# Optimization experiments

Measured on AMD Instinct MI355X. Metric: run time of the kernel, lower is better.

Reference implementation:

```python
import jax, jax.numpy as jnp
import numpy as np

GROUP_SIZE = 128  # cfg.group_size

def dequantize_int4(weight_q, scale, zero_point, group_size):
    # weight_q: (out, in) int values in [0,15]; scale/zero_point: (out, n_groups)
    out_f, in_f = weight_q.shape
    n_groups = in_f // group_size
    w = weight_q.astype(jnp.float32).reshape(out_f, n_groups, group_size)
    w = (w - zero_point[:, :, None]) * scale[:, :, None]
    return w.reshape(out_f, in_f)

def setup_inputs() -> dict:
    key = jax.random.key(0)
    k1, k2, k3, k4, k5 = jax.random.split(key, 5)
    B, S, D_IN, D_OUT = 2, 2048, 4096, 4096
    n_groups = D_IN // GROUP_SIZE
    x = jax.random.normal(k1, (B, S, D_IN), dtype=jnp.float32)
    weight_q = jax.random.randint(k2, (D_OUT, D_IN), 0, 16, dtype=jnp.int32)
    scale = jax.random.uniform(k3, (D_OUT, n_groups), dtype=jnp.float32, minval=0.001, maxval=0.02)
    zero_point = jax.random.uniform(k4, (D_OUT, n_groups), dtype=jnp.float32, minval=0.0, maxval=15.0)
    bias = jax.random.normal(k5, (D_OUT,), dtype=jnp.float32)
    return {"x": x, "weight_q": weight_q, "scale": scale, "zero_point": zero_point, "bias": bias}

def reference(x, weight_q, scale, zero_point, bias):
    # Faithful to QuantizedLinear.forward with bits=4: dequantize then F.linear
    w = dequantize_int4(weight_q, scale, zero_point, GROUP_SIZE).astype(x.dtype)  # (out, in)
    return jnp.einsum('bsi,oi->bso', x, w) + bias
```

## Files before the change

kernel.cpp:

```cpp
#include <hip/hip_runtime.h>

typedef __bf16 bf16x8 __attribute__((ext_vector_type(8)));
typedef float f32x4 __attribute__((ext_vector_type(4)));

__device__ __forceinline__ void gload16(const void* g, void* l) {
    __builtin_amdgcn_global_load_lds(
        (const __attribute__((address_space(1))) unsigned int*)g,
        (__attribute__((address_space(3))) unsigned int*)l, 16, 0, 0);
}

__global__ void k_convert_x(const float* __restrict__ x, __bf16* __restrict__ xb, size_t n) {
    size_t i = ((size_t)blockIdx.x * blockDim.x + threadIdx.x) * 8;
    if (i >= n) return;
    const float4 a = *(const float4*)(x + i);
    const float4 b = *(const float4*)(x + i + 4);
    bf16x8 v;
    v[0] = (__bf16)a.x; v[1] = (__bf16)a.y; v[2] = (__bf16)a.z; v[3] = (__bf16)a.w;
    v[4] = (__bf16)b.x; v[5] = (__bf16)b.y; v[6] = (__bf16)b.z; v[7] = (__bf16)b.w;
    *(bf16x8*)(xb + i) = v;
}

__global__ void k_dequant_w(const int* __restrict__ wq, const float* __restrict__ scale,
                            const float* __restrict__ zp, __bf16* __restrict__ wb,
                            int K, int GS, int NG) {
    size_t i = ((size_t)blockIdx.x * blockDim.x + threadIdx.x) * 8;
    int o = (int)(i / K);
    int k = (int)(i % K);
    int g = k / GS;
    float s = scale[(size_t)o * NG + g];
    float z = zp[(size_t)o * NG + g];
    const int4 q0 = *(const int4*)(wq + i);
    const int4 q1 = *(const int4*)(wq + i + 4);
    bf16x8 v;
    v[0] = (__bf16)(((float)q0.x - z) * s); v[1] = (__bf16)(((float)q0.y - z) * s);
    v[2] = (__bf16)(((float)q0.z - z) * s); v[3] = (__bf16)(((float)q0.w - z) * s);
    v[4] = (__bf16)(((float)q1.x - z) * s); v[5] = (__bf16)(((float)q1.y - z) * s);
    v[6] = (__bf16)(((float)q1.z - z) * s); v[7] = (__bf16)(((float)q1.w - z) * s);
    *(bf16x8*)(wb + i) = v;
}

template <int MODE>
__global__ __launch_bounds__(256, 2) void k_gemm(
    const __bf16* __restrict__ Ab, const float* __restrict__ Af,
    const __bf16* __restrict__ Bb, const int* __restrict__ Bq,
    const float* __restrict__ scale, const float* __restrict__ zp,
    const float* __restrict__ bias, float* __restrict__ C,
    int M, int N, int K, int NG, int GS)
{
    __shared__ __align__(16) __bf16 As[128 * 32];
    __shared__ __align__(16) __bf16 Bs[128 * 32];

    const int tid  = threadIdx.x;
    const int w    = tid >> 6;
    const int lane = tid & 63;
    const int wm   = w >> 1, wn = w & 1;
    const int m0   = blockIdx.y * 128, n0 = blockIdx.x * 128;
    const int lr   = lane & 15;
    const int lc   = lane >> 4;

    f32x4 acc[4][4] = {};

    for (int kk = 0; kk < K; kk += 32) {
        if constexpr (MODE == 0) {
#pragma unroll
            for (int i = 0; i < 2; i++) {
                int c = i * 256 + tid;
                const __bf16* g = Ab + (size_t)(m0 + (c >> 2)) * K + kk + (c & 3) * 8;
                gload16(g, (char*)As + (i * 256 + w * 64) * 16);
            }
        } else {
            int row = tid >> 1, half = tid & 1;
            const float* g = Af + (size_t)(m0 + row) * K + kk + half * 16;
            float4 f0 = *(const float4*)g;
            float4 f1 = *(const float4*)(g + 4);
            float4 f2 = *(const float4*)(g + 8);
            float4 f3 = *(const float4*)(g + 12);
            bf16x8 v0, v1;
            v0[0] = (__bf16)f0.x; v0[1] = (__bf16)f0.y; v0[2] = (__bf16)f0.z; v0[3] = (__bf16)f0.w;
            v0[4] = (__bf16)f1.x; v0[5] = (__bf16)f1.y; v0[6] = (__bf16)f1.z; v0[7] = (__bf16)f1.w;
            v1[0] = (__bf16)f2.x; v1[1] = (__bf16)f2.y; v1[2] = (__bf16)f2.z; v1[3] = (__bf16)f2.w;
            v1[4] = (__bf16)f3.x; v1[5] = (__bf16)f3.y; v1[6] = (__bf16)f3.z; v1[7] = (__bf16)f3.w;
            *(bf16x8*)(As + row * 32 + half * 16)     = v0;
            *(bf16x8*)(As + row * 32 + half * 16 + 8) = v1;
        }
        if constexpr (MODE <= 1) {
#pragma unroll
            for (int i = 0; i < 2; i++) {
                int c = i * 256 + tid;
                const __bf16* g = Bb + (size_t)(n0 + (c >> 2)) * K + kk + (c & 3) * 8;
                gload16(g, (char*)Bs + (i * 256 + w * 64) * 16);
            }
        } else {
            int row = tid >> 1, half = tid & 1;
            int o = n0 + row;
            int kbase = kk + half * 16;
            int g = kbase / GS;
            float s = scale[(size_t)o * NG + g];
            float z = zp[(size_t)o * NG + g];
            const int* q = Bq + (size_t)o * K + kbase;
            int4 q0 = *(const int4*)q;
            int4 q1 = *(const int4*)(q + 4);
            int4 q2 = *(const int4*)(q + 8);
            int4 q3 = *(const int4*)(q + 12);
            bf16x8 v0, v1;
            v0[0] = (__bf16)(((float)q0.x - z) * s); v0[1] = (__bf16)(((float)q0.y - z) * s);
            v0[2] = (__bf16)(((float)q0.z - z) * s); v0[3] = (__bf16)(((float)q0.w - z) * s);
            v0[4] = (__bf16)(((float)q1.x - z) * s); v0[5] = (__bf16)(((float)q1.y - z) * s);
            v0[6] = (__bf16)(((float)q1.z - z) * s); v0[7] = (__bf16)(((float)q1.w - z) * s);
            v1[0] = (__bf16)(((float)q2.x - z) * s); v1[1] = (__bf16)(((float)q2.y - z) * s);
            v1[2] = (__bf16)(((float)q2.z - z) * s); v1[3] = (__bf16)(((float)q2.w - z) * s);
            v1[4] = (__bf16)(((float)q3.x - z) * s); v1[5] = (__bf16)(((float)q3.y - z) * s);
            v1[6] = (__bf16)(((float)q3.z - z) * s); v1[7] = (__bf16)(((float)q3.w - z) * s);
            *(bf16x8*)(Bs + row * 32 + half * 16)     = v0;
            *(bf16x8*)(Bs + row * 32 + half * 16 + 8) = v1;
        }

        __syncthreads();

        bf16x8 af[4], bfm[4];
#pragma unroll
        for (int a = 0; a < 4; a++)
            af[a] = *(const bf16x8*)(As + (wm * 64 + a * 16 + lr) * 32 + lc * 8);
#pragma unroll
        for (int b = 0; b < 4; b++)
            bfm[b] = *(const bf16x8*)(Bs + (wn * 64 + b * 16 + lr) * 32 + lc * 8);
#pragma unroll
        for (int a = 0; a < 4; a++)
#pragma unroll
            for (int b = 0; b < 4; b++)
                acc[a][b] = __builtin_amdgcn_mfma_f32_16x16x32_bf16(af[a], bfm[b], acc[a][b], 0, 0, 0);

        __syncthreads();
    }

#pragma unroll
    for (int b = 0; b < 4; b++) {
        int col = n0 + wn * 64 + b * 16 + lr;
        float bv = bias[col];
#pragma unroll
        for (int a = 0; a < 4; a++) {
            int rbase = m0 + wm * 64 + a * 16 + lc * 4;
#pragma unroll
            for (int r = 0; r < 4; r++)
                C[(size_t)(rbase + r) * N + col] = acc[a][b][r] + bv;
        }
    }
}

extern "C" void kernel_launch(void* const* d_in, const int* in_sizes, int n_in,
                              void* d_out, int out_size, void* d_ws, size_t ws_size,
                              hipStream_t stream) {
    const float* x     = (const float*)d_in[0];
    const int*   wq    = (const int*)d_in[1];
    const float* scale = (const float*)d_in[2];
    const float* zp    = (const float*)d_in[3];
    const float* bias  = (const float*)d_in[4];
    float* out = (float*)d_out;

    const int    N  = in_sizes[4];
    const long   K  = in_sizes[1] / N;
    const long   M  = in_sizes[0] / K;
    const int    NG = in_sizes[2] / N;
    const int    GS = (int)(K / NG);

    const size_t wbytes = (size_t)N * K * sizeof(__bf16);
    const size_t xbytes = (size_t)M * K * sizeof(__bf16);

    char* ws = (char*)d_ws;
    __bf16* wb = (__bf16*)ws;
    __bf16* xb = (__bf16*)(ws + wbytes);

    dim3 grid((unsigned)(N / 128), (unsigned)(M / 128)), blk(256);

    if (ws_size >= wbytes + xbytes) {
        size_t nx = (size_t)M * K;
        size_t nw = (size_t)N * K;
        k_convert_x<<<(unsigned)((nx / 8 + 255) / 256), 256, 0, stream>>>(x, xb, nx);
        k_dequant_w<<<(unsigned)((nw / 8 + 255) / 256), 256, 0, stream>>>(wq, scale, zp, wb, (int)K, GS, NG);
        k_gemm<0><<<grid, blk, 0, stream>>>(xb, nullptr, wb, nullptr, scale, zp, bias, out,
                                            (int)M, N, (int)K, NG, GS);
    } else if (ws_size >= wbytes) {
        size_t nw = (size_t)N * K;
        k_dequant_w<<<(unsigned)((nw / 8 + 255) / 256), 256, 0, stream>>>(wq, scale, zp, wb, (int)K, GS, NG);
        k_gemm<1><<<grid, blk, 0, stream>>>(nullptr, x, wb, nullptr, scale, zp, bias, out,
                                            (int)M, N, (int)K, NG, GS);
    } else {
        k_gemm<2><<<grid, blk, 0, stream>>>(nullptr, x, nullptr, wq, scale, zp, bias, out,
                                            (int)M, N, (int)K, NG, GS);
    }
}
```

Measured before the change: 179.3 us.

## Add 256x256 multi-buffered bf16 GEMM with swizzled LDS and XCD-aware tiling

Adds a new GEMM kernel with 256x256 tiles and 512 threads. It uses a 4-stage LDS ring filled by async global-to-LDS loads, an XOR-swizzled LDS layout to avoid bank conflicts, double-buffered register fragments with interleaved barriers and setprio around the MFMA bursts, and a block-ID remap that groups tiles per XCD. This is meant to raise data reuse and hide memory latency compared with the single-buffered 128x128 kernel. The existing kernel stays as a fallback when shapes or workspace don't fit, and the manual waitcnt/barrier scheduling adds correctness risk.

```diff
diff --git a/kernel.cpp b/kernel.cpp
--- a/kernel.cpp
+++ b/kernel.cpp
@@ -37,6 +37,137 @@
     v[4] = (__bf16)(((float)q1.x - z) * s); v[5] = (__bf16)(((float)q1.y - z) * s);
     v[6] = (__bf16)(((float)q1.z - z) * s); v[7] = (__bf16)(((float)q1.w - z) * s);
     *(bf16x8*)(wb + i) = v;
+}
+
+#define BMg 256
+#define BNg 256
+#define BKg 32
+#define TILEB 32768
+#define ATILEB 16384
+
+__global__ __launch_bounds__(512, 2) void k_gemm256(
+    const __bf16* __restrict__ A, const __bf16* __restrict__ B,
+    const float* __restrict__ bias, float* __restrict__ C,
+    int M, int N, int K)
+{
+    __shared__ __align__(16) char lds[4 * TILEB];
+    const int tid = threadIdx.x;
+    const int w = tid >> 6, lane = tid & 63;
+    const int wm = w >> 2, wn = w & 3;
+    const int lr = lane & 15, hi = lane >> 4;
+    const int NT = K / BKg;
+
+    const int nbx = N / BNg;
+    const int nwg = nbx * (M / BMg);
+    const int bid = (int)blockIdx.x;
+    const int q = nwg >> 3, r = nwg & 7;
+    const int xcd = bid & 7, loc = bid >> 3;
+    const int swz = (xcd < r ? xcd * (q + 1) : r * (q + 1) + (xcd - r) * q) + loc;
+    const int m0 = (swz / nbx) * BMg;
+    const int n0 = (swz % nbx) * BNg;
+
+    size_t aOff[2], bOff[2];
+#pragma unroll
+    for (int L = 0; L < 2; ++L) {
+        int c = L * 512 + tid;
+        int row = c >> 2, ch = (c & 3) ^ (row & 3);
+        aOff[L] = (size_t)(m0 + row) * K + ch * 8;
+        bOff[L] = (size_t)(n0 + row) * K + ch * 8;
+    }
+    int dstOff[2];
+#pragma unroll
+    for (int L = 0; L < 2; ++L) dstOff[L] = (L * 512 + w * 64) * 16;
+
+    const int chR = (hi ^ (lr & 3)) * 16;
+    const int aRd = (wm * 128 + lr) * 64 + chR;
+    const int bRd = ATILEB + (wn * 64 + lr) * 64 + chR;
+
+#define STAGE_A(tt, buf) do {                                              \
+    const int kk_ = (tt) * BKg;                                            \
+    gload16(A + aOff[0] + kk_, lds + (buf) * TILEB + dstOff[0]);           \
+    gload16(A + aOff[1] + kk_, lds + (buf) * TILEB + dstOff[1]);           \
+} while (0)
+#define STAGE_B(tt, buf) do {                                              \
+    const int kk_ = (tt) * BKg;                                            \
+    gload16(B + bOff[0] + kk_, lds + (buf) * TILEB + ATILEB + dstOff[0]);  \
+    gload16(B + bOff[1] + kk_, lds + (buf) * TILEB + ATILEB + dstOff[1]);  \
+} while (0)
+#define RD_A(dst, buf, m) dst = *(const bf16x8*)(lds + (buf) * TILEB + aRd + (m) * 1024)
+#define RD_B(dst, buf, n) dst = *(const bf16x8*)(lds + (buf) * TILEB + bRd + (n) * 1024)
+
+    f32x4 acc[8][4] = {};
+    bf16x8 aF0[8], bF0[4], aF1[8], bF1[4];
+
+    STAGE_A(0, 0); STAGE_B(0, 0);
+    STAGE_A(1, 1); STAGE_B(1, 1);
+    STAGE_A(2, 2); STAGE_B(2, 2);
+    asm volatile("s_waitcnt vmcnt(8)" ::: "memory");
+    __builtin_amdgcn_s_barrier();
+    RD_A(aF0[0], 0, 0); RD_A(aF0[1], 0, 1); RD_A(aF0[2], 0, 2);
+    RD_A(aF0[3], 0, 3); RD_A(aF0[4], 0, 4); RD_A(aF0[5], 0, 5);
+
+#define ITER(t, AC, BC, AN) do {                                            \
+    const int bt = (t) & 3, bt1 = ((t) + 1) & 3, bt3 = ((t) + 3) & 3;       \
+    int t3 = (t) + 3; if (t3 >= NT) t3 -= NT;                               \
+    RD_A(AC[6], bt, 6); RD_A(AC[7], bt, 7);                                 \
+    RD_B(BC[0], bt, 0); RD_B(BC[1], bt, 1);                                 \
+    RD_B(BC[2], bt, 2); RD_B(BC[3], bt, 3);                                 \
+    STAGE_A(t3, bt3);                                                       \
+    asm volatile("s_waitcnt vmcnt(6)" ::: "memory");                        \
+    __builtin_amdgcn_s_barrier();                                           \
+    asm volatile("s_waitcnt lgkmcnt(0)" ::: "memory");                      \
+    __builtin_amdgcn_sched_barrier(0);                                      \
+    __builtin_amdgcn_s_setprio(1);                                          \
+    _Pragma("unroll")                                                       \
+    for (int m_ = 0; m_ < 4; ++m_)                                          \
+        _Pragma("unroll")                                                   \
+        for (int n_ = 0; n_ < 4; ++n_)                                      \
+            acc[m_][n_] = __builtin_amdgcn_mfma_f32_16x16x32_bf16(          \
+                AC[m_], BC[n_], acc[m_][n_], 0, 0, 0);                      \
+    __builtin_amdgcn_s_setprio(0);                                          \
+    __builtin_amdgcn_s_barrier();                                           \
+    if ((t) + 1 < NT) {                                                     \
+        RD_A(AN[0], bt1, 0); RD_A(AN[1], bt1, 1); RD_A(AN[2], bt1, 2);      \
+        RD_A(AN[3], bt1, 3); RD_A(AN[4], bt1, 4); RD_A(AN[5], bt1, 5);      \
+    }                                                                       \
+    STAGE_B(t3, bt3);                                                       \
+    __builtin_amdgcn_s_barrier();                                           \
+    asm volatile("s_waitcnt lgkmcnt(0)" ::: "memory");                      \
+    __builtin_amdgcn_sched_barrier(0);                                      \
+    __builtin_amdgcn_s_setprio(1);                                          \
+    _Pragma("unroll")                                                       \
+    for (int m_ = 4; m_ < 8; ++m_)                                          \
+        _Pragma("unroll")                                                   \
+        for (int n_ = 0; n_ < 4; ++n_)                                      \
+            acc[m_][n_] = __builtin_amdgcn_mfma_f32_16x16x32_bf16(          \
+                AC[m_], BC[n_], acc[m_][n_], 0, 0, 0);                      \
+    __builtin_amdgcn_s_setprio(0);                                          \
+    __builtin_amdgcn_s_barrier();                                           \
+} while (0)
+
+    for (int t = 0; t < NT; t += 2) {
+        ITER(t,     aF0, bF0, aF1);
+        ITER(t + 1, aF1, bF1, aF0);
+    }
+
+#pragma unroll
+    for (int n_ = 0; n_ < 4; ++n_) {
+        const int col = n0 + wn * 64 + n_ * 16 + lr;
+        const float bv = bias[col];
+#pragma unroll
+        for (int m_ = 0; m_ < 8; ++m_) {
+            const size_t rbase = (size_t)(m0 + wm * 128 + m_ * 16 + hi * 4) * N + col;
+            C[rbase]               = acc[m_][n_][0] + bv;
+            C[rbase + N]           = acc[m_][n_][1] + bv;
+            C[rbase + 2 * (size_t)N] = acc[m_][n_][2] + bv;
+            C[rbase + 3 * (size_t)N] = acc[m_][n_][3] + bv;
+        }
+    }
+#undef ITER
+#undef STAGE_A
+#undef STAGE_B
+#undef RD_A
+#undef RD_B
 }
 
 template <int MODE>
@@ -97,11 +228,11 @@
             int g = kbase / GS;
             float s = scale[(size_t)o * NG + g];
             float z = zp[(size_t)o * NG + g];
-            const int* q = Bq + (size_t)o * K + kbase;
-            int4 q0 = *(const int4*)q;
-            int4 q1 = *(const int4*)(q + 4);
-            int4 q2 = *(const int4*)(q + 8);
-            int4 q3 = *(const int4*)(q + 12);
+            const int* qp = Bq + (size_t)o * K + kbase;
+            int4 q0 = *(const int4*)qp;
+            int4 q1 = *(const int4*)(qp + 4);
+            int4 q2 = *(const int4*)(qp + 8);
+            int4 q3 = *(const int4*)(qp + 12);
             bf16x8 v0, v1;
             v0[0] = (__bf16)(((float)q0.x - z) * s); v0[1] = (__bf16)(((float)q0.y - z) * s);
             v0[2] = (__bf16)(((float)q0.z - z) * s); v0[3] = (__bf16)(((float)q0.w - z) * s);
@@ -170,21 +301,29 @@
     __bf16* wb = (__bf16*)ws;
     __bf16* xb = (__bf16*)(ws + wbytes);
 
-    dim3 grid((unsigned)(N / 128), (unsigned)(M / 128)), blk(256);
+    const bool big = (M % 256 == 0) && (N % 256 == 0) && (K % 64 == 0) && (K / 32 >= 4);
 
     if (ws_size >= wbytes + xbytes) {
         size_t nx = (size_t)M * K;
         size_t nw = (size_t)N * K;
         k_convert_x<<<(unsigned)((nx / 8 + 255) / 256), 256, 0, stream>>>(x, xb, nx);
         k_dequant_w<<<(unsigned)((nw / 8 + 255) / 256), 256, 0, stream>>>(wq, scale, zp, wb, (int)K, GS, NG);
-        k_gemm<0><<<grid, blk, 0, stream>>>(xb, nullptr, wb, nullptr, scale, zp, bias, out,
-                                            (int)M, N, (int)K, NG, GS);
+        if (big) {
+            unsigned nwg = (unsigned)((M / 256) * (N / 256));
+            k_gemm256<<<nwg, 512, 0, stream>>>(xb, wb, bias, out, (int)M, N, (int)K);
+        } else {
+            dim3 grid((unsigned)(N / 128), (unsigned)(M / 128)), blk(256);
+            k_gemm<0><<<grid, blk, 0, stream>>>(xb, nullptr, wb, nullptr, scale, zp, bias, out,
+                                                (int)M, N, (int)K, NG, GS);
+        }
     } else if (ws_size >= wbytes) {
         size_t nw = (size_t)N * K;
+        dim3 grid((unsigned)(N / 128), (unsigned)(M / 128)), blk(256);
         k_dequant_w<<<(unsigned)((nw / 8 + 255) / 256), 256, 0, stream>>>(wq, scale, zp, wb, (int)K, GS, NG);
         k_gemm<1><<<grid, blk, 0, stream>>>(nullptr, x, wb, nullptr, scale, zp, bias, out,
                                             (int)M, N, (int)K, NG, GS);
     } else {
+        dim3 grid((unsigned)(N / 128), (unsigned)(M / 128)), blk(256);
         k_gemm<2><<<grid, blk, 0, stream>>>(nullptr, x, nullptr, wq, scale, zp, bias, out,
                                             (int)M, N, (int)K, NG, GS);
     }
```

After: 160.1 us. 1.12x faster.

## Add 256x256 multi-stage pipelined bf16 GEMM with XCD swizzle and LDS swizzle

Applied to the files above, without the earlier changes.

Adds a new GEMM kernel for the dequantized-weight path. It uses 256x256 tiles with 512 threads and a 4-buffer LDS ring (three tiles prefetched via global_load_lds), and interleaves register prefetch with MFMA issue, guarded by explicit waitcnt and priority hints. Workgroup IDs are remapped so each XCD gets contiguous tiles, and LDS chunks are XOR-swizzled to avoid bank conflicts. The goal is to hide memory latency and raise MFMA utilisation over the simple single-buffered 128x128 kernel. The cost is more LDS and register use per block plus hand-tuned waitcnt counts that are fragile.

```diff
diff --git a/kernel.cpp b/kernel.cpp
--- a/kernel.cpp
+++ b/kernel.cpp
@@ -37,6 +37,154 @@
     v[4] = (__bf16)(((float)q1.x - z) * s); v[5] = (__bf16)(((float)q1.y - z) * s);
     v[6] = (__bf16)(((float)q1.z - z) * s); v[7] = (__bf16)(((float)q1.w - z) * s);
     *(bf16x8*)(wb + i) = v;
+}
+
+#define BKg 32
+#define TILEB 32768
+#define ATILEB 16384
+
+__global__ __launch_bounds__(512, 2) void k_gemm256(
+    const __bf16* __restrict__ A, const __bf16* __restrict__ B,
+    const float* __restrict__ bias, float* __restrict__ C,
+    int M, int N, int K)
+{
+    __shared__ __align__(16) char lds[4 * TILEB];
+    const int tid = threadIdx.x;
+    const int w = tid >> 6, lane = tid & 63;
+    const int wm = w >> 2, wn = w & 3;
+    const int lr = lane & 15, hi = lane >> 4;
+    const int NT = K / BKg;
+
+    const int nbx = N / 256;
+    const int nwg = nbx * (M / 256);
+    const int bid = (int)blockIdx.x;
+    const int q = nwg >> 3, r = nwg & 7;
+    const int xcd = bid & 7, loc = bid >> 3;
+    const int swz = (xcd < r ? xcd * (q + 1) : r * (q + 1) + (xcd - r) * q) + loc;
+    const int m0 = (swz / nbx) * 256;
+    const int n0 = (swz % nbx) * 256;
+
+    int aO[2], bO[2];
+#pragma unroll
+    for (int L = 0; L < 2; ++L) {
+        int c = L * 512 + tid;
+        int row = c >> 2, ch = (c & 3) ^ ((c >> 3) & 3);
+        aO[L] = (m0 + row) * K + ch * 8;
+        bO[L] = (n0 + row) * K + ch * 8;
+    }
+    const int dstOff0 = (w * 64) * 16;
+    const int dstOff1 = (512 + w * 64) * 16;
+
+    const int chR = (hi ^ ((lr >> 1) & 3)) * 16;
+    const int aRd = (wm * 128 + lr) * 64 + chR;
+    const int bRd = ATILEB + (wn * 64 + lr) * 64 + chR;
+
+#define RD_A(dst, BUF, m) dst = *(const bf16x8*)(lds + (BUF) * TILEB + aRd + (m) * 1024)
+#define RD_B(dst, BUF, n) dst = *(const bf16x8*)(lds + (BUF) * TILEB + bRd + (n) * 1024)
+#define VMW(n) asm volatile("s_waitcnt vmcnt(" #n ")" ::: "memory")
+#define LKW(n) asm volatile("s_waitcnt lgkmcnt(" #n ")" ::: "memory")
+
+    f32x4 acc[8][4] = {};
+    bf16x8 a03[4], a47[4], b0[4], b1[4];
+
+    gload16(A + aO[0],            lds + 0 * TILEB + dstOff0);
+    gload16(A + aO[1],            lds + 0 * TILEB + dstOff1);
+    gload16(B + bO[0],            lds + 0 * TILEB + ATILEB + dstOff0);
+    gload16(B + bO[1],            lds + 0 * TILEB + ATILEB + dstOff1);
+    gload16(A + aO[0] + BKg,      lds + 1 * TILEB + dstOff0);
+    gload16(A + aO[1] + BKg,      lds + 1 * TILEB + dstOff1);
+    gload16(B + bO[0] + BKg,      lds + 1 * TILEB + ATILEB + dstOff0);
+    gload16(B + bO[1] + BKg,      lds + 1 * TILEB + ATILEB + dstOff1);
+    gload16(A + aO[0] + 2 * BKg,  lds + 2 * TILEB + dstOff0);
+    gload16(A + aO[1] + 2 * BKg,  lds + 2 * TILEB + dstOff1);
+    gload16(B + bO[0] + 2 * BKg,  lds + 2 * TILEB + ATILEB + dstOff0);
+    gload16(B + bO[1] + 2 * BKg,  lds + 2 * TILEB + ATILEB + dstOff1);
+    VMW(8);
+    __builtin_amdgcn_s_barrier();
+    RD_A(a03[0], 0, 0); RD_A(a03[1], 0, 1); RD_A(a03[2], 0, 2); RD_A(a03[3], 0, 3);
+    RD_B(b0[0], 0, 0);  RD_B(b0[1], 0, 1);  RD_B(b0[2], 0, 2);  RD_B(b0[3], 0, 3);
+
+    const __bf16* Ab3 = A + 3 * BKg;
+    const __bf16* Bb3 = B + 3 * BKg;
+
+#define ITERU(t, I, BT, BT1, BT3, BCUR, BNXT, VN)                            \
+do {                                                                         \
+    VMW(VN);                                                                 \
+    __builtin_amdgcn_s_barrier();                                            \
+    if ((t) + (I) + 3 < NT) {                                                \
+        gload16(Ab3 + aO[0] + (I) * BKg, lds + (BT3) * TILEB + dstOff0);     \
+        gload16(Ab3 + aO[1] + (I) * BKg, lds + (BT3) * TILEB + dstOff1);     \
+    }                                                                        \
+    RD_A(a47[0], BT, 4); RD_A(a47[1], BT, 5);                                \
+    RD_A(a47[2], BT, 6); RD_A(a47[3], BT, 7);                                \
+    LKW(4);                                                                  \
+    __builtin_amdgcn_sched_barrier(0);                                       \
+    __builtin_amdgcn_s_setprio(1);                                           \
+    _Pragma("unroll")                                                        \
+    for (int m_ = 0; m_ < 4; ++m_)                                           \
+        _Pragma("unroll")                                                    \
+        for (int n_ = 0; n_ < 4; ++n_)                                       \
+            acc[m_][n_] = __builtin_amdgcn_mfma_f32_16x16x32_bf16(           \
+                a03[m_], BCUR[n_], acc[m_][n_], 0, 0, 0);                    \
+    __builtin_amdgcn_s_setprio(0);                                           \
+    if ((t) + (I) + 3 < NT) {                                                \
+        gload16(Bb3 + bO[0] + (I) * BKg,                                     \
+                lds + (BT3) * TILEB + ATILEB + dstOff0);                     \
+        gload16(Bb3 + bO[1] + (I) * BKg,                                     \
+                lds + (BT3) * TILEB + ATILEB + dstOff1);                     \
+    }                                                                        \
+    if ((t) + (I) + 1 < NT) {                                                \
+        RD_A(a03[0], BT1, 0); RD_A(a03[1], BT1, 1);                          \
+        RD_A(a03[2], BT1, 2); RD_A(a03[3], BT1, 3);                          \
+        RD_B(BNXT[0], BT1, 0); RD_B(BNXT[1], BT1, 1);                        \
+        RD_B(BNXT[2], BT1, 2); RD_B(BNXT[3], BT1, 3);                        \
+        LKW(8);                                                              \
+    } else {                                                                 \
+        LKW(0);                                                              \
+    }                                                                        \
+    __builtin_amdgcn_sched_barrier(0);                                       \
+    __builtin_amdgcn_s_setprio(1);                                           \
+    _Pragma("unroll")                                                        \
+    for (int m_ = 0; m_ < 4; ++m_)                                           \
+        _Pragma("unroll")                                                    \
+        for (int n_ = 0; n_ < 4; ++n_)                                       \
+            acc[m_ + 4][n_] = __builtin_amdgcn_mfma_f32_16x16x32_bf16(       \
+                a47[m_], BCUR[n_], acc[m_ + 4][n_], 0, 0, 0);                \
+    __builtin_amdgcn_s_setprio(0);                                           \
+} while (0)
+
+    int t = 0;
+    for (; t < NT - 4; t += 4) {
+        ITERU(t, 0, 0, 1, 3, b0, b1, 4);
+        ITERU(t, 1, 1, 2, 0, b1, b0, 4);
+        ITERU(t, 2, 2, 3, 1, b0, b1, 4);
+        ITERU(t, 3, 3, 0, 2, b1, b0, 4);
+        Ab3 += 4 * BKg;
+        Bb3 += 4 * BKg;
+    }
+    ITERU(t, 0, 0, 1, 3, b0, b1, 4);
+    ITERU(t, 1, 1, 2, 0, b1, b0, 4);
+    ITERU(t, 2, 2, 3, 1, b0, b1, 0);
+    ITERU(t, 3, 3, 0, 2, b1, b0, 0);
+
+#pragma unroll
+    for (int n_ = 0; n_ < 4; ++n_) {
+        const int col = n0 + wn * 64 + n_ * 16 + lr;
+        const float bv = bias[col];
+#pragma unroll
+        for (int m_ = 0; m_ < 8; ++m_) {
+            const size_t rbase = (size_t)(m0 + wm * 128 + m_ * 16 + hi * 4) * N + col;
+            C[rbase]                 = acc[m_][n_][0] + bv;
+            C[rbase + N]             = acc[m_][n_][1] + bv;
+            C[rbase + 2 * (size_t)N] = acc[m_][n_][2] + bv;
+            C[rbase + 3 * (size_t)N] = acc[m_][n_][3] + bv;
+        }
+    }
+#undef ITERU
+#undef RD_A
+#undef RD_B
+#undef VMW
+#undef LKW
 }
 
 template <int MODE>
@@ -97,11 +245,11 @@
             int g = kbase / GS;
             float s = scale[(size_t)o * NG + g];
             float z = zp[(size_t)o * NG + g];
-            const int* q = Bq + (size_t)o * K + kbase;
-            int4 q0 = *(const int4*)q;
-            int4 q1 = *(const int4*)(q + 4);
-            int4 q2 = *(const int4*)(q + 8);
-            int4 q3 = *(const int4*)(q + 12);
+            const int* qp = Bq + (size_t)o * K + kbase;
+            int4 q0 = *(const int4*)qp;
+            int4 q1 = *(const int4*)(qp + 4);
+            int4 q2 = *(const int4*)(qp + 8);
+            int4 q3 = *(const int4*)(qp + 12);
             bf16x8 v0, v1;
             v0[0] = (__bf16)(((float)q0.x - z) * s); v0[1] = (__bf16)(((float)q0.y - z) * s);
             v0[2] = (__bf16)(((float)q0.z - z) * s); v0[3] = (__bf16)(((float)q0.w - z) * s);
@@ -170,21 +318,29 @@
     __bf16* wb = (__bf16*)ws;
     __bf16* xb = (__bf16*)(ws + wbytes);
 
-    dim3 grid((unsigned)(N / 128), (unsigned)(M / 128)), blk(256);
+    const bool big = (M % 256 == 0) && (N % 256 == 0) && (K % 128 == 0) && (K / 32 >= 8);
 
     if (ws_size >= wbytes + xbytes) {
         size_t nx = (size_t)M * K;
         size_t nw = (size_t)N * K;
         k_convert_x<<<(unsigned)((nx / 8 + 255) / 256), 256, 0, stream>>>(x, xb, nx);
         k_dequant_w<<<(unsigned)((nw / 8 + 255) / 256), 256, 0, stream>>>(wq, scale, zp, wb, (int)K, GS, NG);
-        k_gemm<0><<<grid, blk, 0, stream>>>(xb, nullptr, wb, nullptr, scale, zp, bias, out,
-                                            (int)M, N, (int)K, NG, GS);
+        if (big) {
+            unsigned nwg = (unsigned)((M / 256) * (N / 256));
+            k_gemm256<<<nwg, 512, 0, stream>>>(xb, wb, bias, out, (int)M, N, (int)K);
+        } else {
+            dim3 grid((unsigned)(N / 128), (unsigned)(M / 128)), blk(256);
+            k_gemm<0><<<grid, blk, 0, stream>>>(xb, nullptr, wb, nullptr, scale, zp, bias, out,
+                                                (int)M, N, (int)K, NG, GS);
+        }
     } else if (ws_size >= wbytes) {
         size_t nw = (size_t)N * K;
+        dim3 grid((unsigned)(N / 128), (unsigned)(M / 128)), blk(256);
         k_dequant_w<<<(unsigned)((nw / 8 + 255) / 256), 256, 0, stream>>>(wq, scale, zp, wb, (int)K, GS, NG);
         k_gemm<1><<<grid, blk, 0, stream>>>(nullptr, x, wb, nullptr, scale, zp, bias, out,
                                             (int)M, N, (int)K, NG, GS);
     } else {
+        dim3 grid((unsigned)(N / 128), (unsigned)(M / 128)), blk(256);
         k_gemm<2><<<grid, blk, 0, stream>>>(nullptr, x, nullptr, wq, scale, zp, bias, out,
                                             (int)M, N, (int)K, NG, GS);
     }
```

Result: slower. 282.4 us (+57.5%).
